# Optimization experiments

Hardware: AMD Instinct MI355X
Metric: run time of the kernel (lower is better)

## Reference

```python
import jax, jax.numpy as jnp
import numpy as np

BN_EPS = 1e-5

def conv1x1(x, w, b):
    # x: [B,C,H,W], w: [O,C], b: [O] -> [B,O,H,W]
    return jnp.einsum('bchw,oc->bohw', x, w) + b[None, :, None, None]

def maxpool2x2(x):
    B, C, H, W = x.shape
    return x.reshape(B, C, H // 2, 2, W // 2, 2).max(axis=(3, 5))

def setup_inputs() -> dict:
    key = jax.random.key(0)
    ks = jax.random.split(key, 8)
    B, C, Ci, H, W = 16, 256, 128, 64, 64
    s_in = np.sqrt(2.0 / C).astype(np.float32)   # kaiming fan_out-ish scale
    s_out = np.sqrt(2.0 / Ci).astype(np.float32)
    return {
        'inp0': jax.random.normal(ks[0], (1,), jnp.float32),
        'x': jax.random.normal(ks[1], (B, C, H, W), jnp.float32),
        'g_w': jax.random.normal(ks[2], (Ci, C), jnp.float32) * s_in,
        'g_b': jnp.zeros((Ci,), jnp.float32),
        'theta_w': jax.random.normal(ks[3], (Ci, C), jnp.float32) * s_in,
        'theta_b': jnp.zeros((Ci,), jnp.float32),
        'phi_w': jax.random.normal(ks[4], (Ci, C), jnp.float32) * s_in,
        'phi_b': jnp.zeros((Ci,), jnp.float32),
        'W_w': jax.random.normal(ks[5], (C, Ci), jnp.float32) * s_out,
        'W_b': jnp.zeros((C,), jnp.float32),
        'bn_gamma': jnp.ones((C,), jnp.float32),
        'bn_beta': jnp.zeros((C,), jnp.float32),
    }

def reference(inp0, x, g_w, g_b, theta_w, theta_b, phi_w, phi_b, W_w, W_b, bn_gamma, bn_beta):
    B, C, H, W = x.shape
    Ci = g_w.shape[0]
    # g and phi are conv1x1 followed by 2x2 maxpool (sub_sample=True)
    g_x = maxpool2x2(conv1x1(x, g_w, g_b)).reshape(B, Ci, -1)        # [B,Ci,N']
    g_x = g_x.transpose(0, 2, 1)                                      # [B,N',Ci]
    theta_x = conv1x1(x, theta_w, theta_b).reshape(B, Ci, -1)         # [B,Ci,N]
    theta_x = theta_x.transpose(0, 2, 1)                              # [B,N,Ci]
    phi_x = maxpool2x2(conv1x1(x, phi_w, phi_b)).reshape(B, Ci, -1)   # [B,Ci,N']
    f = jnp.einsum('bnc,bcm->bnm', theta_x, phi_x)                    # [B,N,N'] (no scaling)
    f_div_C = jax.nn.softmax(f, axis=-1)
    y = jnp.einsum('bnm,bmc->bnc', f_div_C, g_x)                      # [B,N,Ci]
    y = y.transpose(0, 2, 1).reshape(B, Ci, H, W)
    W_y = conv1x1(y, W_w, W_b)                                        # [B,C,H,W]
    # BatchNorm2d in training mode: batch statistics (biased var), eps=1e-5
    mean = W_y.mean(axis=(0, 2, 3))
    var = W_y.var(axis=(0, 2, 3))
    W_y = (W_y - mean[None, :, None, None]) * jax.lax.rsqrt(var + BN_EPS)[None, :, None, None]
    W_y = W_y * bn_gamma[None, :, None, None] + bn_beta[None, :, None, None]
    z = W_y + x
    # original returns list(inputs[:index]) + [z] + list(inputs[index+1:])
    return (inp0, z)
```

## Files before the change

### kernel.cpp

```cpp
#include <hip/hip_runtime.h>
#include <stdint.h>

typedef __attribute__((ext_vector_type(4))) float f32x4;
typedef __attribute__((ext_vector_type(8))) short s16x8;

__device__ __forceinline__ unsigned short bf16_rne(float f) {
    union { float f; unsigned u; } v; v.f = f;
    return (unsigned short)((v.u + 0x7fffu + ((v.u >> 16) & 1u)) >> 16);
}
__device__ __forceinline__ float bf16_to_f32(unsigned short h) {
    union { unsigned u; float f; } v; v.u = ((unsigned)h) << 16;
    return v.f;
}

__device__ __forceinline__ void async_copy16(unsigned short* lds, const unsigned short* glb) {
    __builtin_amdgcn_global_load_lds(
        (const __attribute__((address_space(1))) unsigned int*)(glb),
        (__attribute__((address_space(3))) unsigned int*)(lds),
        16, 0, 0);
}


template<int MODE>
__global__ __launch_bounds__(256) void conv_kernel(
    const float* __restrict__ x,
    const float* __restrict__ w,
    const float* __restrict__ bias,
    unsigned short* __restrict__ outH,
    unsigned short* __restrict__ outL)
{
    const int b   = blockIdx.y;
    const int n0  = blockIdx.x * 128;
    const int tid = threadIdx.x;
    const int wv  = tid >> 6;
    const int l   = tid & 63;
    const int lg  = l >> 4;
    const int lc  = l & 15;

    __shared__ __align__(16) unsigned short Ah[128][40];
    __shared__ __align__(16) unsigned short Al[128][40];

    f32x4 acc[8][2];
#pragma unroll
    for (int i = 0; i < 8; i++)
#pragma unroll
        for (int j = 0; j < 2; j++) acc[i][j] = (f32x4){0.f, 0.f, 0.f, 0.f};

    for (int kc = 0; kc < 256; kc += 32) {
        __syncthreads();
#pragma unroll
        for (int i = 0; i < 8; i++) {
            int lin = i * 256 + tid;
            int cp  = lin >> 7;
            int nn  = lin & 127;
            const float* xp = x + ((size_t)b * 256 + (kc + 2 * cp)) * 4096 + n0 + nn;
            float v0 = xp[0];
            float v1 = xp[4096];
            unsigned short h0 = bf16_rne(v0), h1 = bf16_rne(v1);
            *(unsigned*)&Ah[nn][2 * cp] = (unsigned)h0 | ((unsigned)h1 << 16);
            if (MODE != 2) {
                unsigned short l0 = bf16_rne(v0 - bf16_to_f32(h0));
                unsigned short l1 = bf16_rne(v1 - bf16_to_f32(h1));
                *(unsigned*)&Al[nn][2 * cp] = (unsigned)l0 | ((unsigned)l1 << 16);
            }
        }
        __syncthreads();

        s16x8 wh[2], wl[2];
#pragma unroll
        for (int ot = 0; ot < 2; ot++) {
            int orow = wv * 32 + ot * 16 + lc;
            const float* wp = w + (size_t)orow * 256 + kc + lg * 8;
#pragma unroll
            for (int j = 0; j < 8; j++) {
                float wvv = wp[j];
                unsigned short h = bf16_rne(wvv);
                wh[ot][j] = (short)h;
                if (MODE != 2) wl[ot][j] = (short)bf16_rne(wvv - bf16_to_f32(h));
            }
        }

#pragma unroll
        for (int mt = 0; mt < 8; mt++) {
            s16x8 ah = *(const s16x8*)&Ah[mt * 16 + lc][lg * 8];
            s16x8 al;
            if (MODE != 2) al = *(const s16x8*)&Al[mt * 16 + lc][lg * 8];
#pragma unroll
            for (int ot = 0; ot < 2; ot++) {
                acc[mt][ot] = __builtin_amdgcn_mfma_f32_16x16x32_bf16(ah, wh[ot], acc[mt][ot], 0, 0, 0);
                if (MODE != 2) {
                    acc[mt][ot] = __builtin_amdgcn_mfma_f32_16x16x32_bf16(ah, wl[ot], acc[mt][ot], 0, 0, 0);
                    acc[mt][ot] = __builtin_amdgcn_mfma_f32_16x16x32_bf16(al, wh[ot], acc[mt][ot], 0, 0, 0);
                }
            }
        }
    }

    if (MODE == 0) {
#pragma unroll
        for (int mt = 0; mt < 8; mt++)
#pragma unroll
            for (int ot = 0; ot < 2; ot++) {
                int o = wv * 32 + ot * 16 + lc;
                float bs = bias[o];
#pragma unroll
                for (int r = 0; r < 4; r++) {
                    int n = n0 + mt * 16 + lg * 4 + r;
                    float v = acc[mt][ot][r] + bs;
                    unsigned short h = bf16_rne(v);
                    size_t idx = ((size_t)b * 4096 + n) * 128 + o;
                    outH[idx] = h;
                    outL[idx] = bf16_rne(v - bf16_to_f32(h));
                }
            }
    } else {
        const int mbase = blockIdx.x * 32;
#pragma unroll
        for (int mt = 0; mt < 4; mt++)
#pragma unroll
            for (int ot = 0; ot < 2; ot++) {
                int o = wv * 32 + ot * 16 + lc;
                float bs = bias[o];
#pragma unroll
                for (int pair = 0; pair < 2; pair++) {
                    float v = fmaxf(fmaxf(acc[mt][ot][2 * pair], acc[mt][ot][2 * pair + 1]),
                                    fmaxf(acc[mt + 4][ot][2 * pair], acc[mt + 4][ot][2 * pair + 1])) + bs;
                    int pw = mt * 8 + lg * 2 + pair;
                    int m  = mbase + pw;
                    if (MODE == 1) {
                        unsigned short h = bf16_rne(v);
                        size_t idx = ((size_t)b * 1024 + m) * 128 + o;
                        outH[idx] = h;
                        outL[idx] = bf16_rne(v - bf16_to_f32(h));
                    } else {
                        outH[((size_t)b * 128 + o) * 1024 + m] = bf16_rne(v);
                    }
                }
            }
    }
}

__global__ __launch_bounds__(256, 4) void attn_kernel(
    const unsigned short* __restrict__ thH,
    const unsigned short* __restrict__ thL,
    const unsigned short* __restrict__ phH,
    const unsigned short* __restrict__ phL,
    const unsigned short* __restrict__ gp,
    unsigned short* __restrict__ y)
{
    const int fid  = blockIdx.x + (blockIdx.y << 6);
    const int xcd  = fid & 7;
    const int slot = fid >> 3;
    const int b    = 2 * xcd + (slot >> 6);
    const int n0   = (slot & 63) * 64;

    const int tid = threadIdx.x;
    const int wv  = tid >> 6;
    const int l   = tid & 63;
    const int lg  = l >> 4;
    const int lc  = l & 15;

    __shared__ __align__(16) unsigned short Kh[2][32 * 128];
    __shared__ __align__(16) unsigned short Kl[2][32 * 128];
    __shared__ __align__(16) unsigned short Pb[4][16 * 40];

    const unsigned short* phHb = phH + (size_t)b * 1024 * 128;
    const unsigned short* phLb = phL + (size_t)b * 1024 * 128;
    const unsigned short* gpb  = gp  + (size_t)b * 128 * 1024;
    unsigned short* Pw = Pb[wv];

    s16x8 qh[4], ql[4];
    {
        const size_t qrow = ((size_t)b * 4096 + n0 + wv * 16 + lc) * 128;
#pragma unroll
        for (int ks = 0; ks < 4; ks++) {
            qh[ks] = *(const s16x8*)(thH + qrow + ks * 32 + lg * 8);
            ql[ks] = *(const s16x8*)(thL + qrow + ks * 32 + lg * 8);
        }
    }

    f32x4 O[8];
#pragma unroll
    for (int t = 0; t < 8; t++) O[t] = (f32x4){0.f, 0.f, 0.f, 0.f};
    float mrun = -1e30f;
    float lrun = 0.f;

    const int lr  = l >> 4;
    const int sc_ = l & 15;

#define STAGE(buf, kt_)                                                              \
    {                                                                                \
        _Pragma("unroll")                                                            \
        for (int t = 0; t < 2; t++) {                                                \
            int Rt = wv * 8 + t * 4;                                                 \
            int R  = Rt + lr;                                                        \
            int ck = sc_ ^ (R & 15);                                                 \
            size_t src = ((size_t)((kt_) * 32 + R)) * 128 + ck * 8;                  \
            async_copy16(&Kh[buf][Rt * 128], phHb + src);                            \
            async_copy16(&Kl[buf][Rt * 128], phLb + src);                            \
        }                                                                            \
    }

    STAGE(0, 0);

    for (int kt = 0; kt < 32; kt++) {
        const int cur = kt & 1;
        __syncthreads();
        if (kt < 31) STAGE(cur ^ 1, kt + 1);

        const unsigned short* KhT = Kh[cur];
        const unsigned short* KlT = Kl[cur];

        f32x4 s[2];
#pragma unroll
        for (int ct = 0; ct < 2; ct++) s[ct] = (f32x4){0.f, 0.f, 0.f, 0.f};
#pragma unroll
        for (int ct = 0; ct < 2; ct++) {
            const int row = ct * 16 + lc;
#pragma unroll
            for (int ks = 0; ks < 4; ks++) {
                const int slt = (ks * 4 + lg) ^ lc;
                s16x8 kh = *(const s16x8*)(KhT + row * 128 + slt * 8);
                s16x8 kl = *(const s16x8*)(KlT + row * 128 + slt * 8);
                s[ct] = __builtin_amdgcn_mfma_f32_16x16x32_bf16(kh, qh[ks], s[ct], 0, 0, 0);
                s[ct] = __builtin_amdgcn_mfma_f32_16x16x32_bf16(kl, qh[ks], s[ct], 0, 0, 0);
                s[ct] = __builtin_amdgcn_mfma_f32_16x16x32_bf16(kh, ql[ks], s[ct], 0, 0, 0);
            }
        }

        float tm = fmaxf(fmaxf(fmaxf(s[0][0], s[0][1]), fmaxf(s[0][2], s[0][3])),
                         fmaxf(fmaxf(s[1][0], s[1][1]), fmaxf(s[1][2], s[1][3])));
        tm = fmaxf(tm, __shfl_xor(tm, 16, 64));
        tm = fmaxf(tm, __shfl_xor(tm, 32, 64));

        if (__any(tm > mrun)) {
            float mn  = fmaxf(mrun, tm);
            float scr = __expf(mrun - mn);
            mrun = mn;
            lrun *= scr;
            float scO[4];
#pragma unroll
            for (int r = 0; r < 4; r++) scO[r] = __shfl(scr, lg * 4 + r, 64);
#pragma unroll
            for (int t = 0; t < 8; t++)
#pragma unroll
                for (int r = 0; r < 4; r++) O[t][r] *= scO[r];
        }

        float ts = 0.f;
        float p[8];
#pragma unroll
        for (int ct = 0; ct < 2; ct++)
#pragma unroll
            for (int r = 0; r < 4; r++) {
                float e = __expf(s[ct][r] - mrun);
                p[ct * 4 + r] = e;
                ts += e;
            }
        ts += __shfl_xor(ts, 16, 64);
        ts += __shfl_xor(ts, 32, 64);
        lrun += ts;

#pragma unroll
        for (int ct = 0; ct < 2; ct++) {
            unsigned w0 = (unsigned)bf16_rne(p[ct * 4 + 0]) | ((unsigned)bf16_rne(p[ct * 4 + 1]) << 16);
            unsigned w1 = (unsigned)bf16_rne(p[ct * 4 + 2]) | ((unsigned)bf16_rne(p[ct * 4 + 3]) << 16);
            uint2 pk; pk.x = w0; pk.y = w1;
            *(uint2*)&Pw[lc * 40 + ct * 16 + lg * 4] = pk;
        }

        const int mt = kt * 32;
        s16x8 pa = *(const s16x8*)(Pw + lc * 40 + lg * 8);
#pragma unroll
        for (int ci_t = 0; ci_t < 8; ci_t++) {
            s16x8 vb = *(const s16x8*)(gpb + (size_t)(ci_t * 16 + lc) * 1024 + mt + lg * 8);
            O[ci_t] = __builtin_amdgcn_mfma_f32_16x16x32_bf16(pa, vb, O[ci_t], 0, 0, 0);
        }
    }

    float invO[4];
#pragma unroll
    for (int r = 0; r < 4; r++) {
        float lr_ = __shfl(lrun, lg * 4 + r, 64);
        invO[r] = 1.0f / lr_;
    }
#pragma unroll
    for (int r = 0; r < 4; r++) {
        int n = n0 + wv * 16 + lg * 4 + r;
        size_t base = ((size_t)b * 4096 + n) * 128;
#pragma unroll
        for (int ci_t = 0; ci_t < 8; ci_t++)
            y[base + ci_t * 16 + lc] = bf16_rne(O[ci_t][r] * invO[r]);
    }
#undef STAGE
}

__global__ __launch_bounds__(256) void wconv_kernel(
    const unsigned short* __restrict__ y,
    const float* __restrict__ Ww,
    const float* __restrict__ Wb,
    unsigned short* __restrict__ wy)
{
    const int b   = blockIdx.z;
    const int o0  = blockIdx.x * 64;
    const int nb  = blockIdx.y * 256;
    const int tid = threadIdx.x;
    const int wv  = tid >> 6;
    const int l   = tid & 63;
    const int lg  = l >> 4;
    const int lc  = l & 15;
    const int n0  = nb + wv * 64;

    f32x4 acc[4][4];
#pragma unroll
    for (int i = 0; i < 4; i++)
#pragma unroll
        for (int j = 0; j < 4; j++) acc[i][j] = (f32x4){0.f, 0.f, 0.f, 0.f};

#pragma unroll
    for (int ks = 0; ks < 4; ks++) {
        s16x8 a[4];
#pragma unroll
        for (int ot = 0; ot < 4; ot++) {
            const float* wp = Ww + (size_t)(o0 + ot * 16 + lc) * 128 + ks * 32 + lg * 8;
#pragma unroll
            for (int j = 0; j < 8; j++) a[ot][j] = (short)bf16_rne(wp[j]);
        }
#pragma unroll
        for (int nt = 0; nt < 4; nt++) {
            s16x8 bf = *(const s16x8*)(y + ((size_t)b * 4096 + n0 + nt * 16 + lc) * 128 + ks * 32 + lg * 8);
#pragma unroll
            for (int ot = 0; ot < 4; ot++)
                acc[ot][nt] = __builtin_amdgcn_mfma_f32_16x16x32_bf16(a[ot], bf, acc[ot][nt], 0, 0, 0);
        }
    }
#pragma unroll
    for (int ot = 0; ot < 4; ot++) {
#pragma unroll
        for (int r = 0; r < 4; r++) {
            int o = o0 + ot * 16 + lg * 4 + r;
            float bsv = Wb[o];
#pragma unroll
            for (int nt = 0; nt < 4; nt++) {
                float v = acc[ot][nt][r] + bsv;
                wy[((size_t)b * 256 + o) * 4096 + n0 + nt * 16 + lc] = bf16_rne(v);
            }
        }
    }
}

__global__ __launch_bounds__(256) void stats_kernel(
    const unsigned short* __restrict__ wy,
    const float* __restrict__ gamma, const float* __restrict__ beta,
    float* __restrict__ scale, float* __restrict__ shift)
{
    const int o = blockIdx.x;
    const int t = threadIdx.x;
    float s1 = 0.f, s2 = 0.f;
    for (int b = 0; b < 16; b++) {
        const unsigned short* p = wy + ((size_t)b * 256 + o) * 4096;
#pragma unroll
        for (int i = 0; i < 4; i++) {
            uint2 u = *(const uint2*)(p + i * 1024 + t * 4);
            float v0 = bf16_to_f32((unsigned short)(u.x & 0xffff));
            float v1 = bf16_to_f32((unsigned short)(u.x >> 16));
            float v2 = bf16_to_f32((unsigned short)(u.y & 0xffff));
            float v3 = bf16_to_f32((unsigned short)(u.y >> 16));
            s1 += v0 + v1 + v2 + v3;
            s2 += v0 * v0 + v1 * v1 + v2 * v2 + v3 * v3;
        }
    }
#pragma unroll
    for (int d = 1; d < 64; d <<= 1) { s1 += __shfl_xor(s1, d, 64); s2 += __shfl_xor(s2, d, 64); }
    __shared__ float rs1[4], rs2[4];
    if ((t & 63) == 0) { rs1[t >> 6] = s1; rs2[t >> 6] = s2; }
    __syncthreads();
    if (t == 0) {
        float S1 = rs1[0] + rs1[1] + rs1[2] + rs1[3];
        float S2 = rs2[0] + rs2[1] + rs2[2] + rs2[3];
        const float cnt = 16.0f * 4096.0f;
        float mean = S1 / cnt;
        float var  = S2 / cnt - mean * mean;
        float sc = gamma[o] * rsqrtf(var + 1e-5f);
        scale[o] = sc;
        shift[o] = beta[o] - mean * sc;
    }
}

__global__ __launch_bounds__(256) void final_kernel(
    const unsigned short* __restrict__ wy,
    const float* __restrict__ x,
    const float* __restrict__ scale, const float* __restrict__ shift,
    const float* __restrict__ inp0,
    float* __restrict__ out)
{
    if (blockIdx.x == 0 && threadIdx.x == 0) out[0] = inp0[0];
    float* z = out + 1;
    const size_t total4 = (size_t)16 * 256 * 4096 / 4;
    for (size_t v = (size_t)blockIdx.x * 256 + threadIdx.x; v < total4; v += (size_t)gridDim.x * 256) {
        size_t e = v * 4;
        int c = (int)((e >> 12) & 255);
        uint2 u = *(const uint2*)(wy + e);
        float4 xv = *(const float4*)(x + e);
        float sc = scale[c], sh = shift[c];
        float z0 = sc * bf16_to_f32((unsigned short)(u.x & 0xffff)) + sh + xv.x;
        float z1 = sc * bf16_to_f32((unsigned short)(u.x >> 16))    + sh + xv.y;
        float z2 = sc * bf16_to_f32((unsigned short)(u.y & 0xffff)) + sh + xv.z;
        float z3 = sc * bf16_to_f32((unsigned short)(u.y >> 16))    + sh + xv.w;
        z[e + 0] = z0; z[e + 1] = z1; z[e + 2] = z2; z[e + 3] = z3;
    }
}

extern "C" void kernel_launch(void* const* d_in, const int* in_sizes, int n_in,
                              void* d_out, int out_size, void* d_ws, size_t ws_size,
                              hipStream_t stream) {
    const float* inp0  = (const float*)d_in[0];
    const float* x     = (const float*)d_in[1];
    const float* g_w   = (const float*)d_in[2];
    const float* g_b   = (const float*)d_in[3];
    const float* th_w  = (const float*)d_in[4];
    const float* th_b  = (const float*)d_in[5];
    const float* ph_w  = (const float*)d_in[6];
    const float* ph_b  = (const float*)d_in[7];
    const float* W_w   = (const float*)d_in[8];
    const float* W_b   = (const float*)d_in[9];
    const float* gamma = (const float*)d_in[10];
    const float* beta  = (const float*)d_in[11];

    char* ws = (char*)d_ws;
    const size_t MB = 1048576;
    unsigned short* thH = (unsigned short*)(ws);
    unsigned short* thL = (unsigned short*)(ws + 16 * MB);
    unsigned short* phH = (unsigned short*)(ws + 32 * MB);
    unsigned short* phL = (unsigned short*)(ws + 36 * MB);
    unsigned short* gpv = (unsigned short*)(ws + 40 * MB);
    unsigned short* yv  = (unsigned short*)(ws + 44 * MB);
    unsigned short* wy  = (unsigned short*)(ws + 60 * MB);
    float* scaleb       = (float*)(ws + 92 * MB);
    float* shiftb       = (float*)(ws + 92 * MB + 1024);

    conv_kernel<0><<<dim3(32, 16), 256, 0, stream>>>(x, th_w, th_b, thH, thL);
    conv_kernel<1><<<dim3(32, 16), 256, 0, stream>>>(x, ph_w, ph_b, phH, phL);
    conv_kernel<2><<<dim3(32, 16), 256, 0, stream>>>(x, g_w, g_b, gpv, gpv);
    attn_kernel<<<dim3(64, 16), 256, 0, stream>>>(thH, thL, phH, phL, gpv, yv);
    wconv_kernel<<<dim3(4, 16, 16), 256, 0, stream>>>(yv, W_w, W_b, wy);
    stats_kernel<<<dim3(256), 256, 0, stream>>>(wy, gamma, beta, scaleb, shiftb);
    final_kernel<<<dim3(2048), 256, 0, stream>>>(wy, x, scaleb, shiftb, inp0, (float*)d_out);
}
```

Baseline: 402.0 us.

## Pre-split x and weights into transposed bf16 hi/lo buffers once

Adds a kernel that converts x once into transposed [B,N,C] bf16 hi/lo arrays, and another that pre-splits all conv weights (and W_w) into bf16. The three conv kernels then read MFMA fragments straight from global memory instead of each re-reading fp32 x, converting it and staging it through LDS. This removes the redundant conversion work repeated across the three convs, but adds an extra write and read of a 32MB-per-part intermediate and depends on cache hits for the fragment loads. The workspace is reorganised and reused across stages.

```diff
diff --git a/kernel.cpp b/kernel.cpp
--- a/kernel.cpp
+++ b/kernel.cpp
@@ -21,10 +21,75 @@
 }
 
 
+__global__ __launch_bounds__(256) void wsplit_kernel(
+    const float* __restrict__ th_w, const float* __restrict__ ph_w,
+    const float* __restrict__ g_w,  const float* __restrict__ W_w,
+    unsigned short* __restrict__ wH, unsigned short* __restrict__ wL,
+    unsigned short* __restrict__ wbf)
+{
+    int idx = blockIdx.x * 256 + threadIdx.x;
+    if (idx < 98304) {
+        const float* src = (idx < 32768) ? th_w : ((idx < 65536) ? ph_w : g_w);
+        float v = src[idx & 32767];
+        unsigned short h = bf16_rne(v);
+        wH[idx] = h;
+        wL[idx] = bf16_rne(v - bf16_to_f32(h));
+    } else {
+        int off = idx - 98304;
+        wbf[off] = bf16_rne(W_w[off]);
+    }
+}
+
+__global__ __launch_bounds__(256) void xsplit_kernel(
+    const float* __restrict__ x,
+    unsigned short* __restrict__ xtH, unsigned short* __restrict__ xtL)
+{
+    const int b   = blockIdx.y;
+    const int n0  = blockIdx.x * 128;
+    const int tid = threadIdx.x;
+    __shared__ unsigned short Th[128][36];
+    __shared__ unsigned short Tl[128][36];
+    const int row  = tid >> 1;
+    const int half = tid & 1;
+
+    for (int kc = 0; kc < 256; kc += 32) {
+        __syncthreads();
+#pragma unroll
+        for (int i = 0; i < 16; i++) {
+            int lin = i * 256 + tid;
+            int cc = lin >> 7, nn = lin & 127;
+            float v = x[((size_t)b * 256 + kc + cc) * 4096 + n0 + nn];
+            unsigned short h = bf16_rne(v);
+            Th[nn][cc] = h;
+            Tl[nn][cc] = bf16_rne(v - bf16_to_f32(h));
+        }
+        __syncthreads();
+        uint2 a0 = *(const uint2*)&Th[row][half * 16 + 0];
+        uint2 a1 = *(const uint2*)&Th[row][half * 16 + 4];
+        uint2 a2 = *(const uint2*)&Th[row][half * 16 + 8];
+        uint2 a3 = *(const uint2*)&Th[row][half * 16 + 12];
+        uint2 b0 = *(const uint2*)&Tl[row][half * 16 + 0];
+        uint2 b1 = *(const uint2*)&Tl[row][half * 16 + 4];
+        uint2 b2 = *(const uint2*)&Tl[row][half * 16 + 8];
+        uint2 b3 = *(const uint2*)&Tl[row][half * 16 + 12];
+        size_t dst = ((size_t)b * 4096 + n0 + row) * 256 + kc + half * 16;
+        uint4 h0; h0.x = a0.x; h0.y = a0.y; h0.z = a1.x; h0.w = a1.y;
+        uint4 h1; h1.x = a2.x; h1.y = a2.y; h1.z = a3.x; h1.w = a3.y;
+        uint4 l0; l0.x = b0.x; l0.y = b0.y; l0.z = b1.x; l0.w = b1.y;
+        uint4 l1; l1.x = b2.x; l1.y = b2.y; l1.z = b3.x; l1.w = b3.y;
+        *(uint4*)(xtH + dst)     = h0;
+        *(uint4*)(xtH + dst + 8) = h1;
+        *(uint4*)(xtL + dst)     = l0;
+        *(uint4*)(xtL + dst + 8) = l1;
+    }
+}
+
 template<int MODE>
-__global__ __launch_bounds__(256) void conv_kernel(
-    const float* __restrict__ x,
-    const float* __restrict__ w,
+__global__ __launch_bounds__(256, 4) void conv_kernel(
+    const unsigned short* __restrict__ xtH,
+    const unsigned short* __restrict__ xtL,
+    const unsigned short* __restrict__ wHs,
+    const unsigned short* __restrict__ wLs,
     const float* __restrict__ bias,
     unsigned short* __restrict__ outH,
     unsigned short* __restrict__ outL)
@@ -37,54 +102,28 @@
     const int lg  = l >> 4;
     const int lc  = l & 15;
 
-    __shared__ __align__(16) unsigned short Ah[128][40];
-    __shared__ __align__(16) unsigned short Al[128][40];
-
     f32x4 acc[8][2];
 #pragma unroll
     for (int i = 0; i < 8; i++)
 #pragma unroll
         for (int j = 0; j < 2; j++) acc[i][j] = (f32x4){0.f, 0.f, 0.f, 0.f};
 
+    const size_t abase = (size_t)b * 4096 + n0;
+
     for (int kc = 0; kc < 256; kc += 32) {
-        __syncthreads();
-#pragma unroll
-        for (int i = 0; i < 8; i++) {
-            int lin = i * 256 + tid;
-            int cp  = lin >> 7;
-            int nn  = lin & 127;
-            const float* xp = x + ((size_t)b * 256 + (kc + 2 * cp)) * 4096 + n0 + nn;
-            float v0 = xp[0];
-            float v1 = xp[4096];
-            unsigned short h0 = bf16_rne(v0), h1 = bf16_rne(v1);
-            *(unsigned*)&Ah[nn][2 * cp] = (unsigned)h0 | ((unsigned)h1 << 16);
-            if (MODE != 2) {
-                unsigned short l0 = bf16_rne(v0 - bf16_to_f32(h0));
-                unsigned short l1 = bf16_rne(v1 - bf16_to_f32(h1));
-                *(unsigned*)&Al[nn][2 * cp] = (unsigned)l0 | ((unsigned)l1 << 16);
-            }
-        }
-        __syncthreads();
-
         s16x8 wh[2], wl[2];
 #pragma unroll
         for (int ot = 0; ot < 2; ot++) {
-            int orow = wv * 32 + ot * 16 + lc;
-            const float* wp = w + (size_t)orow * 256 + kc + lg * 8;
-#pragma unroll
-            for (int j = 0; j < 8; j++) {
-                float wvv = wp[j];
-                unsigned short h = bf16_rne(wvv);
-                wh[ot][j] = (short)h;
-                if (MODE != 2) wl[ot][j] = (short)bf16_rne(wvv - bf16_to_f32(h));
-            }
-        }
-
+            size_t woff = (size_t)(wv * 32 + ot * 16 + lc) * 256 + kc + lg * 8;
+            wh[ot] = *(const s16x8*)(wHs + woff);
+            if (MODE != 2) wl[ot] = *(const s16x8*)(wLs + woff);
+        }
 #pragma unroll
         for (int mt = 0; mt < 8; mt++) {
-            s16x8 ah = *(const s16x8*)&Ah[mt * 16 + lc][lg * 8];
+            size_t aoff = (abase + mt * 16 + lc) * 256 + kc + lg * 8;
+            s16x8 ah = *(const s16x8*)(xtH + aoff);
             s16x8 al;
-            if (MODE != 2) al = *(const s16x8*)&Al[mt * 16 + lc][lg * 8];
+            if (MODE != 2) al = *(const s16x8*)(xtL + aoff);
 #pragma unroll
             for (int ot = 0; ot < 2; ot++) {
                 acc[mt][ot] = __builtin_amdgcn_mfma_f32_16x16x32_bf16(ah, wh[ot], acc[mt][ot], 0, 0, 0);
@@ -297,7 +336,7 @@
 
 __global__ __launch_bounds__(256) void wconv_kernel(
     const unsigned short* __restrict__ y,
-    const float* __restrict__ Ww,
+    const unsigned short* __restrict__ wbf,
     const float* __restrict__ Wb,
     unsigned short* __restrict__ wy)
 {
@@ -321,11 +360,8 @@
     for (int ks = 0; ks < 4; ks++) {
         s16x8 a[4];
 #pragma unroll
-        for (int ot = 0; ot < 4; ot++) {
-            const float* wp = Ww + (size_t)(o0 + ot * 16 + lc) * 128 + ks * 32 + lg * 8;
-#pragma unroll
-            for (int j = 0; j < 8; j++) a[ot][j] = (short)bf16_rne(wp[j]);
-        }
+        for (int ot = 0; ot < 4; ot++)
+            a[ot] = *(const s16x8*)(wbf + (size_t)(o0 + ot * 16 + lc) * 128 + ks * 32 + lg * 8);
 #pragma unroll
         for (int nt = 0; nt < 4; nt++) {
             s16x8 bf = *(const s16x8*)(y + ((size_t)b * 4096 + n0 + nt * 16 + lc) * 128 + ks * 32 + lg * 8);
@@ -429,21 +465,28 @@
 
     char* ws = (char*)d_ws;
     const size_t MB = 1048576;
-    unsigned short* thH = (unsigned short*)(ws);
-    unsigned short* thL = (unsigned short*)(ws + 16 * MB);
-    unsigned short* phH = (unsigned short*)(ws + 32 * MB);
-    unsigned short* phL = (unsigned short*)(ws + 36 * MB);
-    unsigned short* gpv = (unsigned short*)(ws + 40 * MB);
-    unsigned short* yv  = (unsigned short*)(ws + 44 * MB);
-    unsigned short* wy  = (unsigned short*)(ws + 60 * MB);
-    float* scaleb       = (float*)(ws + 92 * MB);
-    float* shiftb       = (float*)(ws + 92 * MB + 1024);
-
-    conv_kernel<0><<<dim3(32, 16), 256, 0, stream>>>(x, th_w, th_b, thH, thL);
-    conv_kernel<1><<<dim3(32, 16), 256, 0, stream>>>(x, ph_w, ph_b, phH, phL);
-    conv_kernel<2><<<dim3(32, 16), 256, 0, stream>>>(x, g_w, g_b, gpv, gpv);
+    unsigned short* xtH = (unsigned short*)(ws);
+    unsigned short* xtL = (unsigned short*)(ws + 32 * MB);
+    unsigned short* thH = (unsigned short*)(ws + 64 * MB);
+    unsigned short* thL = (unsigned short*)(ws + 80 * MB);
+    unsigned short* phH = (unsigned short*)(ws + 96 * MB);
+    unsigned short* phL = (unsigned short*)(ws + 100 * MB);
+    unsigned short* gpv = (unsigned short*)(ws + 104 * MB);
+    unsigned short* wHs = (unsigned short*)(ws + 108 * MB);
+    unsigned short* wLs = (unsigned short*)(ws + 109 * MB);
+    unsigned short* wbf = (unsigned short*)(ws + 110 * MB);
+    float* scaleb       = (float*)(ws + 111 * MB);
+    float* shiftb       = (float*)(ws + 111 * MB + 4096);
+    unsigned short* yv  = (unsigned short*)(ws + 32 * MB);
+    unsigned short* wy  = (unsigned short*)(ws);
+
+    wsplit_kernel<<<dim3(512), 256, 0, stream>>>(th_w, ph_w, g_w, W_w, wHs, wLs, wbf);
+    xsplit_kernel<<<dim3(32, 16), 256, 0, stream>>>(x, xtH, xtL);
+    conv_kernel<0><<<dim3(32, 16), 256, 0, stream>>>(xtH, xtL, wHs,         wLs,         th_b, thH, thL);
+    conv_kernel<1><<<dim3(32, 16), 256, 0, stream>>>(xtH, xtL, wHs + 32768, wLs + 32768, ph_b, phH, phL);
+    conv_kernel<2><<<dim3(32, 16), 256, 0, stream>>>(xtH, xtL, wHs + 65536, wHs + 65536, g_b,  gpv, gpv);
     attn_kernel<<<dim3(64, 16), 256, 0, stream>>>(thH, thL, phH, phL, gpv, yv);
-    wconv_kernel<<<dim3(4, 16, 16), 256, 0, stream>>>(yv, W_w, W_b, wy);
+    wconv_kernel<<<dim3(4, 16, 16), 256, 0, stream>>>(yv, wbf, W_b, wy);
     stats_kernel<<<dim3(256), 256, 0, stream>>>(wy, gamma, beta, scaleb, shiftb);
     final_kernel<<<dim3(2048), 256, 0, stream>>>(wy, x, scaleb, shiftb, inp0, (float*)d_out);
 }
```

Result: slower. 534.2 us (+32.9%).
